# Kernel tuning notes

Hardware: AMD Instinct MI355X
Metric: run time of the kernel (lower is better)

## Reference

```python
import jax, jax.numpy as jnp
import numpy as np

EPS = 1e-5
NH, NS = 8, 4


def layer_norm(x, g, b):
    m = jnp.mean(x, axis=-1, keepdims=True)
    v = jnp.mean((x - m) ** 2, axis=-1, keepdims=True)
    return (x - m) * jax.lax.rsqrt(v + EPS) * g + b


def grid_sample_border(feat, grid):
    # feat: (B,C,H,W), grid: (B,P,S,2) with (x,y) in [-1,1]; bilinear,
    # padding_mode='border', align_corners=True (matches F.grid_sample).
    B, C, H, W = feat.shape
    gx = jnp.clip((grid[..., 0] + 1.0) * 0.5 * (W - 1), 0.0, W - 1.0)
    gy = jnp.clip((grid[..., 1] + 1.0) * 0.5 * (H - 1), 0.0, H - 1.0)
    x0 = jnp.floor(gx)
    y0 = jnp.floor(gy)
    wx = (gx - x0)[:, None]  # (B,1,P,S)
    wy = (gy - y0)[:, None]
    x0i = x0.astype(jnp.int32)
    y0i = y0.astype(jnp.int32)
    x1i = jnp.minimum(x0i + 1, W - 1)
    y1i = jnp.minimum(y0i + 1, H - 1)
    ff = feat.reshape(B, C, H * W)
    gather = jax.vmap(lambda f, i: f[:, i])  # per-batch gather -> (B,C,P,S)
    v00 = gather(ff, y0i * W + x0i)
    v01 = gather(ff, y0i * W + x1i)
    v10 = gather(ff, y1i * W + x0i)
    v11 = gather(ff, y1i * W + x1i)
    return (v00 * (1 - wx) * (1 - wy) + v01 * wx * (1 - wy)
            + v10 * (1 - wx) * wy + v11 * wx * wy)


def setup_inputs() -> dict:
    key = jax.random.key(0)
    ks = jax.random.split(key, 32)
    dim, base = 256, 64
    hd = dim // NH
    inp = {
        'x': jax.random.normal(ks[0], (4, 6, 1024, dim), jnp.float32),
        'ref': jax.random.uniform(ks[1], (4, 1024, 2), jnp.float32) * 2.0 - 1.0,
        'feat0': jax.random.normal(ks[2], (4, base, 128, 128), jnp.float32),
        'feat1': jax.random.normal(ks[3], (4, base * 2, 64, 64), jnp.float32),
        'feat2': jax.random.normal(ks[4], (4, base * 4, 32, 32), jnp.float32),
        'feat3': jax.random.normal(ks[5], (4, base * 8, 16, 16), jnp.float32),
        'feat4': jax.random.normal(ks[6], (4, dim, 16, 16), jnp.float32),
        'norm1_g': jnp.ones((dim,), jnp.float32),
        'norm1_b': jnp.zeros((dim,), jnp.float32),
        'aw_W': 0.02 * jax.random.normal(ks[7], (dim, NH * NS), jnp.float32),
        'aw_b': 0.02 * jax.random.normal(ks[8], (NH * NS,), jnp.float32),
        'so_W': 0.02 * jax.random.normal(ks[9], (dim, 2 * NH * NS), jnp.float32),
        'so_b': 0.1 * jax.random.normal(ks[10], (2 * NH * NS,), jnp.float32),
        'ep0_W': 0.02 * jax.random.normal(ks[11], (base, hd), jnp.float32),
        'ep0_b': jnp.zeros((hd,), jnp.float32),
        'ep1_W': 0.02 * jax.random.normal(ks[12], (base * 2, hd), jnp.float32),
        'ep1_b': jnp.zeros((hd,), jnp.float32),
        'ep2_W': 0.02 * jax.random.normal(ks[13], (base * 4, hd), jnp.float32),
        'ep2_b': jnp.zeros((hd,), jnp.float32),
        'ep3_W': 0.02 * jax.random.normal(ks[14], (base * 8, hd), jnp.float32),
        'ep3_b': jnp.zeros((hd,), jnp.float32),
        'ep4_W': 0.02 * jax.random.normal(ks[15], (dim, hd), jnp.float32),
        'ep4_b': jnp.zeros((hd,), jnp.float32),
        'norm2_g': jnp.ones((dim,), jnp.float32),
        'norm2_b': jnp.zeros((dim,), jnp.float32),
        'fc1_W': 0.02 * jax.random.normal(ks[16], (dim, 2 * dim), jnp.float32),
        'fc1_b': jnp.zeros((2 * dim,), jnp.float32),
        'fc2_W': 0.02 * jax.random.normal(ks[17], (2 * dim, dim), jnp.float32),
        'fc2_b': jnp.zeros((dim,), jnp.float32),
    }
    return inp


def reference(x, ref, feat0, feat1, feat2, feat3, feat4,
              norm1_g, norm1_b, aw_W, aw_b, so_W, so_b,
              ep0_W, ep0_b, ep1_W, ep1_b, ep2_W, ep2_b, ep3_W, ep3_b, ep4_W, ep4_b,
              norm2_g, norm2_b, fc1_W, fc1_b, fc2_W, fc2_b):
    x0_tok, xq = x[:, :1], x[:, 1:]
    b, l, p, c = xq.shape
    hd = c // NH
    residual = xq
    h = layer_norm(xq + x0_tok, norm1_g, norm1_b)
    weights = jax.nn.softmax((h @ aw_W + aw_b).reshape(b, l, p, NH, NS), axis=-1)
    offsets = jnp.tanh((h @ so_W + so_b).reshape(b, l, p, NH * NS, 2))
    pos = offsets + ref[:, None, :, None, :]  # (b,l,p,S,2)
    feats = [feat0, feat1, feat2, feat3, feat4]
    eps_ = [(ep0_W, ep0_b), (ep1_W, ep1_b), (ep2_W, ep2_b), (ep3_W, ep3_b), (ep4_W, ep4_b)]
    sampled = []
    for idx in range(l):
        s = grid_sample_border(feats[idx], pos[:, idx])  # (b,C,p,S)
        s = jnp.transpose(s, (0, 2, 3, 1))                # (b,p,S,C)
        Wp, bp = eps_[idx]
        sampled.append(s @ Wp + bp)                       # (b,p,S,hd)
    fs = jnp.stack(sampled, axis=1).reshape(b, l, p, NH, NS, hd)
    out = jnp.einsum('blphs,blphsd->blphd', weights, fs).reshape(b, l, p, c)
    xq2 = residual + out
    h2 = layer_norm(xq2, norm2_g, norm2_b)
    mlp = jax.nn.gelu(h2 @ fc1_W + fc1_b, approximate=False) @ fc2_W + fc2_b
    xq2 = xq2 + mlp
    return jnp.concatenate([x0_tok, xq2], axis=1)
```

## Files before the change

### kernel.cpp

```cpp
#include <hip/hip_runtime.h>
#include <math.h>

#define B_ 4
#define L_ 5
#define P_ 1024
#define C_ 256
#define TOK (B_ * L_ * P_)

#define PF0_S 0u
#define PF1_S 2097152u
#define PF2_S 2621440u
#define PF3_S 2752512u
#define PF4_S 2785280u
#define WTS_F 1409024u
#define POSS_F 2064384u
#define U_S   0u
#define H1_S  10485760u
#define S_S   15728640u
#define WC_S  17694720u
#define W1T_S 17719296u
#define W2T_S 17850368u
#define BCAT_F 8990720u
#define EWT_S  17981824u

typedef short bf16x8 __attribute__((ext_vector_type(8)));
typedef float f32x4  __attribute__((ext_vector_type(4)));

__device__ __forceinline__ unsigned short f2bf(float f) {
  unsigned u = __float_as_uint(f);
  unsigned r = (u + 0x7fffu + ((u >> 16) & 1u)) >> 16;
  return (unsigned short)r;
}
__device__ __forceinline__ float bf2f(unsigned short u) {
  return __uint_as_float((unsigned)u << 16);
}

__global__ void copy_x0(const float* __restrict__ x, float* __restrict__ out) {
  int i = blockIdx.x * 256 + threadIdx.x;
  int b = i / (P_ * C_);
  int r = i - b * (P_ * C_);
  size_t off = (size_t)b * 6 * P_ * C_ + r;
  out[off] = x[off];
}

__device__ __forceinline__ void block_stats(float v, float* ra, float* rb,
                                            int tid, float* mean, float* var) {
  float a = v, s2 = v * v;
  #pragma unroll
  for (int off = 32; off > 0; off >>= 1) {
    a  += __shfl_xor(a, off);
    s2 += __shfl_xor(s2, off);
  }
  if ((tid & 63) == 0) { ra[tid >> 6] = a; rb[tid >> 6] = s2; }
  __syncthreads();
  float s  = ra[0] + ra[1] + ra[2] + ra[3];
  float ss = rb[0] + rb[1] + rb[2] + rb[3];
  float m = s * (1.0f / C_);
  *mean = m;
  *var = ss * (1.0f / C_) - m * m;
}

__global__ void ln1_h(const float* __restrict__ x,
                      const float* __restrict__ g, const float* __restrict__ bt,
                      unsigned short* __restrict__ h1) {
  __shared__ float ra[4], rb[4];
  int t = blockIdx.x;
  int b = t / (L_ * P_);
  int r = t - b * (L_ * P_);
  int l = r >> 10;
  int p = r & 1023;
  int c = threadIdx.x;
  size_t xq_off = (((size_t)b * 6 + (l + 1)) * P_ + p) * C_;
  size_t x0_off = (((size_t)b * 6) * P_ + p) * C_;
  float v = x[xq_off + c] + x[x0_off + c];
  float mean, var;
  block_stats(v, ra, rb, c, &mean, &var);
  float h = (v - mean) * rsqrtf(var + 1e-5f) * g[c] + bt[c];
  h1[(size_t)t * C_ + c] = f2bf(h);
}

__global__ void ln2_h(const float* __restrict__ out,
                      const float* __restrict__ g, const float* __restrict__ bt,
                      unsigned short* __restrict__ h2) {
  __shared__ float ra[4], rb[4];
  int t = blockIdx.x;
  int b = t / (L_ * P_);
  int r = t - b * (L_ * P_);
  int l = r >> 10;
  int p = r & 1023;
  int c = threadIdx.x;
  size_t o = (((size_t)b * 6 + (l + 1)) * P_ + p) * C_;
  float v = out[o + c];
  float mean, var;
  block_stats(v, ra, rb, c, &mean, &var);
  float h = (v - mean) * rsqrtf(var + 1e-5f) * g[c] + bt[c];
  h2[(size_t)t * C_ + c] = f2bf(h);
}

__global__ void prep_all(const float* __restrict__ f1W, const float* __restrict__ f2W,
                         const float* __restrict__ awW, const float* __restrict__ soW,
                         const float* __restrict__ awb, const float* __restrict__ sob,
                         const float* __restrict__ e0W, const float* __restrict__ e1W,
                         const float* __restrict__ e2W, const float* __restrict__ e3W,
                         const float* __restrict__ e4W,
                         unsigned short* __restrict__ W1T, unsigned short* __restrict__ W2T,
                         unsigned short* __restrict__ Wc, unsigned short* __restrict__ eWT,
                         float* __restrict__ bcat) {
  int i = blockIdx.x * 256 + threadIdx.x;
  if (i < 131072) {
    int n = i >> 8, k = i & 255;
    W1T[i] = f2bf(f1W[k * 512 + n]);
  } else if (i < 262144) {
    int j = i - 131072;
    int n = j >> 9, k = j & 511;
    W2T[j] = f2bf(f2W[k * 256 + n]);
  } else if (i < 286720) {
    int j = i - 262144;
    int n = j >> 8, k = j & 255;
    Wc[j] = f2bf(n < 32 ? awW[k * 32 + n] : soW[k * 64 + (n - 32)]);
  } else if (i < 325632) {
    int j = i - 286720;
    const float* eW; int Cl, base, jj;
    if (j < 2048)       { eW = e0W; Cl = 64;  base = 0;     jj = j; }
    else if (j < 6144)  { eW = e1W; Cl = 128; base = 2048;  jj = j - 2048; }
    else if (j < 14336) { eW = e2W; Cl = 256; base = 6144;  jj = j - 6144; }
    else if (j < 30720) { eW = e3W; Cl = 512; base = 14336; jj = j - 14336; }
    else                { eW = e4W; Cl = 256; base = 30720; jj = j - 30720; }
    int d = jj / Cl, c = jj & (Cl - 1);
    eWT[base + jj] = f2bf(eW[c * 32 + d]);
  } else if (i < 325728) {
    int j = i - 325632;
    bcat[j] = j < 32 ? awb[j] : sob[j - 32];
  }
}

__global__ __launch_bounds__(256) void proj_gemm(
    const float* __restrict__ f0, const float* __restrict__ f1,
    const float* __restrict__ f2, const float* __restrict__ f3,
    const float* __restrict__ f4,
    const unsigned short* __restrict__ eWT,
    unsigned short* __restrict__ pf) {
  constexpr int LDK = 72;
  __shared__ unsigned short Al[64 * LDK];
  __shared__ unsigned short Bl[32 * LDK];
  int blk = blockIdx.x, tid = threadIdx.x;

  const float* feat; int Cl, HW, lt; unsigned pfo, eo;
  if (blk < 1024)      { feat = f0; Cl = 64;  HW = 16384; pfo = PF0_S; eo = 0;     lt = blk; }
  else if (blk < 1280) { feat = f1; Cl = 128; HW = 4096;  pfo = PF1_S; eo = 2048;  lt = blk - 1024; }
  else if (blk < 1344) { feat = f2; Cl = 256; HW = 1024;  pfo = PF2_S; eo = 6144;  lt = blk - 1280; }
  else if (blk < 1360) { feat = f3; Cl = 512; HW = 256;   pfo = PF3_S; eo = 14336; lt = blk - 1344; }
  else                 { feat = f4; Cl = 256; HW = 256;   pfo = PF4_S; eo = 30720; lt = blk - 1360; }
  int tpb = HW >> 6;
  int b = lt / tpb;
  int hw0 = (lt - b * tpb) * 64;
  const float* fb = feat + (size_t)b * Cl * HW;

  int cl = tid & 63, quad = tid >> 6;
  int w = tid >> 6, lane = tid & 63, q = lane >> 4, ml = lane & 15;

  f32x4 acc0 = (f32x4){0.f, 0.f, 0.f, 0.f};
  f32x4 acc1 = (f32x4){0.f, 0.f, 0.f, 0.f};

  for (int k0 = 0; k0 < Cl; k0 += 64) {
    if (k0) __syncthreads();
    { int rr = tid >> 3, kc = (tid & 7) * 8;
      *(int4*)(Bl + rr * LDK + kc) = *(const int4*)(eWT + eo + (size_t)rr * Cl + k0 + kc); }
    const float* src = fb + (size_t)(k0 + cl) * HW + hw0 + quad * 16;
    float4 v0 = *(const float4*)(src);
    float4 v1 = *(const float4*)(src + 4);
    float4 v2 = *(const float4*)(src + 8);
    float4 v3 = *(const float4*)(src + 12);
    unsigned short* ac = Al + cl;
    int mb = quad * 16;
    ac[(mb + 0)  * LDK] = f2bf(v0.x); ac[(mb + 1)  * LDK] = f2bf(v0.y);
    ac[(mb + 2)  * LDK] = f2bf(v0.z); ac[(mb + 3)  * LDK] = f2bf(v0.w);
    ac[(mb + 4)  * LDK] = f2bf(v1.x); ac[(mb + 5)  * LDK] = f2bf(v1.y);
    ac[(mb + 6)  * LDK] = f2bf(v1.z); ac[(mb + 7)  * LDK] = f2bf(v1.w);
    ac[(mb + 8)  * LDK] = f2bf(v2.x); ac[(mb + 9)  * LDK] = f2bf(v2.y);
    ac[(mb + 10) * LDK] = f2bf(v2.z); ac[(mb + 11) * LDK] = f2bf(v2.w);
    ac[(mb + 12) * LDK] = f2bf(v3.x); ac[(mb + 13) * LDK] = f2bf(v3.y);
    ac[(mb + 14) * LDK] = f2bf(v3.z); ac[(mb + 15) * LDK] = f2bf(v3.w);
    __syncthreads();
    #pragma unroll
    for (int ks = 0; ks < 2; ks++) {
      bf16x8 af = *(const bf16x8*)(Al + (w * 16 + ml) * LDK + ks * 32 + q * 8);
      bf16x8 b0 = *(const bf16x8*)(Bl + ml * LDK + ks * 32 + q * 8);
      bf16x8 b1 = *(const bf16x8*)(Bl + (16 + ml) * LDK + ks * 32 + q * 8);
      acc0 = __builtin_amdgcn_mfma_f32_16x16x32_bf16(af, b0, acc0, 0, 0, 0);
      acc1 = __builtin_amdgcn_mfma_f32_16x16x32_bf16(af, b1, acc1, 0, 0, 0);
    }
  }

  #pragma unroll
  for (int nt = 0; nt < 2; nt++) {
    f32x4 a = nt ? acc1 : acc0;
    int d = nt * 16 + ml;
    #pragma unroll
    for (int rr = 0; rr < 4; rr++) {
      int m = w * 16 + q * 4 + rr;
      pf[pfo + ((size_t)b * HW + hw0 + m) * 32 + d] = f2bf(a[rr]);
    }
  }
}

__global__ void postproc(const unsigned short* __restrict__ S, const float* __restrict__ ref,
                         float* __restrict__ wts, float* __restrict__ poss) {
  int t = blockIdx.x;
  int c = threadIdx.x;
  int b = t / (L_ * P_);
  int p = t & (P_ - 1);
  if (c < 32) {
    int g4 = (c >> 2) << 2;
    float s0 = bf2f(S[(size_t)t * 96 + g4 + 0]);
    float s1 = bf2f(S[(size_t)t * 96 + g4 + 1]);
    float s2 = bf2f(S[(size_t)t * 96 + g4 + 2]);
    float s3 = bf2f(S[(size_t)t * 96 + g4 + 3]);
    float m = fmaxf(fmaxf(s0, s1), fmaxf(s2, s3));
    float den = expf(s0 - m) + expf(s1 - m) + expf(s2 - m) + expf(s3 - m);
    float sc = bf2f(S[(size_t)t * 96 + c]);
    wts[(size_t)t * 32 + c] = expf(sc - m) / den;
  } else if (c < 96) {
    int j = c - 32;
    float sv = bf2f(S[(size_t)t * 96 + 32 + j]);
    poss[(size_t)t * 64 + j] = tanhf(sv) + ref[((size_t)b * P_ + p) * 2 + (j & 1)];
  }
}

__global__ __launch_bounds__(256) void sample_comb(
    const float* __restrict__ x, const unsigned short* __restrict__ pf,
    const float* __restrict__ wts, const float* __restrict__ poss,
    const float* __restrict__ e0b, const float* __restrict__ e1b,
    const float* __restrict__ e2b, const float* __restrict__ e3b,
    const float* __restrict__ e4b,
    float* __restrict__ out) {
  __shared__ float coef[512];
  __shared__ int   hwid[512];
  int blk = blockIdx.x;
  int t0 = blk * 4;
  int b = t0 / (L_ * P_);
  int r = t0 - b * (L_ * P_);
  int l = r >> 10;
  int p0 = r & 1023;
  int tid = threadIdx.x;

  int Hl; unsigned pfo; const float* eb;
  if (l == 0)      { Hl = 128; pfo = PF0_S; eb = e0b; }
  else if (l == 1) { Hl = 64;  pfo = PF1_S; eb = e1b; }
  else if (l == 2) { Hl = 32;  pfo = PF2_S; eb = e2b; }
  else if (l == 3) { Hl = 16;  pfo = PF3_S; eb = e3b; }
  else             { Hl = 16;  pfo = PF4_S; eb = e4b; }

  if (tid < 128) {
    int tl = tid >> 5, s = tid & 31;
    int t = t0 + tl;
    float aw = wts[(size_t)t * 32 + s];
    float px = poss[(size_t)t * 64 + s * 2 + 0];
    float py = poss[(size_t)t * 64 + s * 2 + 1];
    float Wm = (float)(Hl - 1);
    float gx = fminf(fmaxf((px + 1.0f) * 0.5f * Wm, 0.0f), Wm);
    float gy = fminf(fmaxf((py + 1.0f) * 0.5f * Wm, 0.0f), Wm);
    float x0f = floorf(gx), y0f = floorf(gy);
    int x0 = (int)x0f, y0 = (int)y0f;
    int x1 = min(x0 + 1, Hl - 1), y1 = min(y0 + 1, Hl - 1);
    float wx = gx - x0f, wy = gy - y0f;
    int base = tid * 4;
    hwid[base + 0] = y0 * Hl + x0; coef[base + 0] = aw * (1.f - wx) * (1.f - wy);
    hwid[base + 1] = y0 * Hl + x1; coef[base + 1] = aw * wx * (1.f - wy);
    hwid[base + 2] = y1 * Hl + x0; coef[base + 2] = aw * (1.f - wx) * wy;
    hwid[base + 3] = y1 * Hl + x1; coef[base + 3] = aw * wx * wy;
  }
  __syncthreads();

  int h = tid >> 5, d = tid & 31;
  const unsigned short* pfb = pf + pfo + (size_t)b * (Hl * Hl) * 32;
  float bv = eb[d];
  #pragma unroll
  for (int tk = 0; tk < 4; ++tk) {
    int cb = tk * 128 + h * 16;
    float acc = 0.f;
    #pragma unroll
    for (int k = 0; k < 16; ++k)
      acc += coef[cb + k] * bf2f(pfb[(size_t)hwid[cb + k] * 32 + d]);
    int p = p0 + tk;
    size_t o = (((size_t)b * 6 + l + 1) * P_ + p) * C_ + h * 32 + d;
    out[o] = x[o] + acc + bv;
  }
}

template<int MODE>
__global__ __launch_bounds__(256) void gemm_bf16(
    const unsigned short* __restrict__ A, const unsigned short* __restrict__ Bt,
    const float* __restrict__ bias, unsigned short* __restrict__ outU,
    float* __restrict__ outF, int N, int K) {
  constexpr int LDK = 72;
  __shared__ unsigned short Al[64 * LDK];
  __shared__ unsigned short Bl[64 * LDK];
  int m0 = blockIdx.x * 64, n0 = blockIdx.y * 64;
  int tid = threadIdx.x;
  int w = tid >> 6, lane = tid & 63;
  int q = lane >> 4, ml = lane & 15;
  int lr = tid >> 3;
  int lk = (tid & 7) * 8;

  f32x4 acc[4];
  #pragma unroll
  for (int i = 0; i < 4; i++) acc[i] = (f32x4){0.f, 0.f, 0.f, 0.f};

  int nr0 = min(n0 + lr, N - 1);
  int nr1 = min(n0 + 32 + lr, N - 1);

  for (int k0 = 0; k0 < K; k0 += 64) {
    int4 a0 = *(const int4*)(A + (size_t)(m0 + lr) * K + k0 + lk);
    int4 a1 = *(const int4*)(A + (size_t)(m0 + 32 + lr) * K + k0 + lk);
    int4 b0 = *(const int4*)(Bt + (size_t)nr0 * K + k0 + lk);
    int4 b1 = *(const int4*)(Bt + (size_t)nr1 * K + k0 + lk);
    __syncthreads();
    *(int4*)(Al + lr * LDK + lk) = a0;
    *(int4*)(Al + (32 + lr) * LDK + lk) = a1;
    *(int4*)(Bl + lr * LDK + lk) = b0;
    *(int4*)(Bl + (32 + lr) * LDK + lk) = b1;
    __syncthreads();
    #pragma unroll
    for (int ks = 0; ks < 2; ks++) {
      bf16x8 af = *(const bf16x8*)(Al + (w * 16 + ml) * LDK + ks * 32 + q * 8);
      #pragma unroll
      for (int nt = 0; nt < 4; nt++) {
        bf16x8 bf = *(const bf16x8*)(Bl + (nt * 16 + ml) * LDK + ks * 32 + q * 8);
        acc[nt] = __builtin_amdgcn_mfma_f32_16x16x32_bf16(af, bf, acc[nt], 0, 0, 0);
      }
    }
  }

  #pragma unroll
  for (int nt = 0; nt < 4; nt++) {
    int n = n0 + nt * 16 + ml;
    if (n >= N) continue;
    float bv = bias[n];
    #pragma unroll
    for (int rr = 0; rr < 4; rr++) {
      int m = m0 + w * 16 + q * 4 + rr;
      float v = acc[nt][rr] + bv;
      if (MODE == 0) {
        v = 0.5f * v * (1.0f + erff(v * 0.70710678118654752f));
        outU[(size_t)m * N + n] = f2bf(v);
      } else if (MODE == 2) {
        outU[(size_t)m * N + n] = f2bf(v);
      } else {
        int s = m >> 10;
        int p = m & 1023;
        int bb = s / 5, ll = s - bb * 5;
        size_t o = (((size_t)bb * 6 + ll + 1) * P_ + p) * C_ + n;
        outF[o] += v;
      }
    }
  }
}

extern "C" void kernel_launch(void* const* d_in, const int* in_sizes, int n_in,
                              void* d_out, int out_size, void* d_ws, size_t ws_size,
                              hipStream_t stream) {
  const float* x     = (const float*)d_in[0];
  const float* ref   = (const float*)d_in[1];
  const float* feat0 = (const float*)d_in[2];
  const float* feat1 = (const float*)d_in[3];
  const float* feat2 = (const float*)d_in[4];
  const float* feat3 = (const float*)d_in[5];
  const float* feat4 = (const float*)d_in[6];
  const float* n1g   = (const float*)d_in[7];
  const float* n1b   = (const float*)d_in[8];
  const float* awW   = (const float*)d_in[9];
  const float* awb   = (const float*)d_in[10];
  const float* soW   = (const float*)d_in[11];
  const float* sob   = (const float*)d_in[12];
  const float* e0W   = (const float*)d_in[13];
  const float* e0b   = (const float*)d_in[14];
  const float* e1W   = (const float*)d_in[15];
  const float* e1b   = (const float*)d_in[16];
  const float* e2W   = (const float*)d_in[17];
  const float* e2b   = (const float*)d_in[18];
  const float* e3W   = (const float*)d_in[19];
  const float* e3b   = (const float*)d_in[20];
  const float* e4W   = (const float*)d_in[21];
  const float* e4b   = (const float*)d_in[22];
  const float* n2g   = (const float*)d_in[23];
  const float* n2b   = (const float*)d_in[24];
  const float* f1W   = (const float*)d_in[25];
  const float* f1b   = (const float*)d_in[26];
  const float* f2W   = (const float*)d_in[27];
  const float* f2b   = (const float*)d_in[28];

  float* wsf = (float*)d_ws;
  unsigned short* ws16 = (unsigned short*)d_ws;
  unsigned short* pf  = ws16;
  float* wts  = wsf + WTS_F;
  float* poss = wsf + POSS_F;
  unsigned short* u   = ws16 + U_S;
  unsigned short* h1  = ws16 + H1_S;
  unsigned short* S   = ws16 + S_S;
  unsigned short* Wc  = ws16 + WC_S;
  unsigned short* W1T = ws16 + W1T_S;
  unsigned short* W2T = ws16 + W2T_S;
  unsigned short* eWT = ws16 + EWT_S;
  float* bcat = wsf + BCAT_F;
  float* out = (float*)d_out;

  prep_all<<<1273, 256, 0, stream>>>(f1W, f2W, awW, soW, awb, sob,
                                     e0W, e1W, e2W, e3W, e4W,
                                     W1T, W2T, Wc, eWT, bcat);

  proj_gemm<<<1376, 256, 0, stream>>>(feat0, feat1, feat2, feat3, feat4, eWT, pf);

  copy_x0<<<(B_ * P_ * C_) / 256, 256, 0, stream>>>(x, out);

  ln1_h<<<TOK, 256, 0, stream>>>(x, n1g, n1b, h1);

  gemm_bf16<2><<<dim3(320, 2), 256, 0, stream>>>(h1, Wc, bcat, S, nullptr, 96, 256);

  postproc<<<TOK, 128, 0, stream>>>(S, ref, wts, poss);

  sample_comb<<<TOK / 4, 256, 0, stream>>>(x, pf, wts, poss,
                                           e0b, e1b, e2b, e3b, e4b, out);

  ln2_h<<<TOK, 256, 0, stream>>>(out, n2g, n2b, h1);

  gemm_bf16<0><<<dim3(320, 8), 256, 0, stream>>>(h1, W1T, f1b, u, nullptr, 512, 256);

  gemm_bf16<1><<<dim3(320, 4), 256, 0, stream>>>(u, W2T, f2b, nullptr, out, 256, 512);
}
```

Baseline: 256.8 us.

## Fuse LN1 with attention projection GEMM and softmax/tanh, and sampling with LN2

```diff
diff --git a/kernel.cpp b/kernel.cpp
--- a/kernel.cpp
+++ b/kernel.cpp
@@ -15,8 +15,7 @@
 #define WTS_F 1409024u
 #define POSS_F 2064384u
 #define U_S   0u
-#define H1_S  10485760u
-#define S_S   15728640u
+#define H2_S  10485760u
 #define WC_S  17694720u
 #define W1T_S 17719296u
 #define W2T_S 17850368u
@@ -35,69 +34,8 @@
   return __uint_as_float((unsigned)u << 16);
 }
 
-__global__ void copy_x0(const float* __restrict__ x, float* __restrict__ out) {
-  int i = blockIdx.x * 256 + threadIdx.x;
-  int b = i / (P_ * C_);
-  int r = i - b * (P_ * C_);
-  size_t off = (size_t)b * 6 * P_ * C_ + r;
-  out[off] = x[off];
-}
-
-__device__ __forceinline__ void block_stats(float v, float* ra, float* rb,
-                                            int tid, float* mean, float* var) {
-  float a = v, s2 = v * v;
-  #pragma unroll
-  for (int off = 32; off > 0; off >>= 1) {
-    a  += __shfl_xor(a, off);
-    s2 += __shfl_xor(s2, off);
-  }
-  if ((tid & 63) == 0) { ra[tid >> 6] = a; rb[tid >> 6] = s2; }
-  __syncthreads();
-  float s  = ra[0] + ra[1] + ra[2] + ra[3];
-  float ss = rb[0] + rb[1] + rb[2] + rb[3];
-  float m = s * (1.0f / C_);
-  *mean = m;
-  *var = ss * (1.0f / C_) - m * m;
-}
-
-__global__ void ln1_h(const float* __restrict__ x,
-                      const float* __restrict__ g, const float* __restrict__ bt,
-                      unsigned short* __restrict__ h1) {
-  __shared__ float ra[4], rb[4];
-  int t = blockIdx.x;
-  int b = t / (L_ * P_);
-  int r = t - b * (L_ * P_);
-  int l = r >> 10;
-  int p = r & 1023;
-  int c = threadIdx.x;
-  size_t xq_off = (((size_t)b * 6 + (l + 1)) * P_ + p) * C_;
-  size_t x0_off = (((size_t)b * 6) * P_ + p) * C_;
-  float v = x[xq_off + c] + x[x0_off + c];
-  float mean, var;
-  block_stats(v, ra, rb, c, &mean, &var);
-  float h = (v - mean) * rsqrtf(var + 1e-5f) * g[c] + bt[c];
-  h1[(size_t)t * C_ + c] = f2bf(h);
-}
-
-__global__ void ln2_h(const float* __restrict__ out,
-                      const float* __restrict__ g, const float* __restrict__ bt,
-                      unsigned short* __restrict__ h2) {
-  __shared__ float ra[4], rb[4];
-  int t = blockIdx.x;
-  int b = t / (L_ * P_);
-  int r = t - b * (L_ * P_);
-  int l = r >> 10;
-  int p = r & 1023;
-  int c = threadIdx.x;
-  size_t o = (((size_t)b * 6 + (l + 1)) * P_ + p) * C_;
-  float v = out[o + c];
-  float mean, var;
-  block_stats(v, ra, rb, c, &mean, &var);
-  float h = (v - mean) * rsqrtf(var + 1e-5f) * g[c] + bt[c];
-  h2[(size_t)t * C_ + c] = f2bf(h);
-}
-
-__global__ void prep_all(const float* __restrict__ f1W, const float* __restrict__ f2W,
+__global__ void prep_all(const float* __restrict__ x, float* __restrict__ out,
+                         const float* __restrict__ f1W, const float* __restrict__ f2W,
                          const float* __restrict__ awW, const float* __restrict__ soW,
                          const float* __restrict__ awb, const float* __restrict__ sob,
                          const float* __restrict__ e0W, const float* __restrict__ e1W,
@@ -107,6 +45,14 @@
                          unsigned short* __restrict__ Wc, unsigned short* __restrict__ eWT,
                          float* __restrict__ bcat) {
   int i = blockIdx.x * 256 + threadIdx.x;
+  if (i < 1048576) {
+    int b = i >> 18;
+    int r = i & 262143;
+    size_t off = (size_t)b * 6 * P_ * C_ + r;
+    out[off] = x[off];
+    return;
+  }
+  i -= 1048576;
   if (i < 131072) {
     int n = i >> 8, k = i & 255;
     W1T[i] = f2bf(f1W[k * 512 + n]);
@@ -204,44 +150,128 @@
   }
 }
 
-__global__ void postproc(const unsigned short* __restrict__ S, const float* __restrict__ ref,
-                         float* __restrict__ wts, float* __restrict__ poss) {
-  int t = blockIdx.x;
-  int c = threadIdx.x;
-  int b = t / (L_ * P_);
-  int p = t & (P_ - 1);
-  if (c < 32) {
-    int g4 = (c >> 2) << 2;
-    float s0 = bf2f(S[(size_t)t * 96 + g4 + 0]);
-    float s1 = bf2f(S[(size_t)t * 96 + g4 + 1]);
-    float s2 = bf2f(S[(size_t)t * 96 + g4 + 2]);
-    float s3 = bf2f(S[(size_t)t * 96 + g4 + 3]);
-    float m = fmaxf(fmaxf(s0, s1), fmaxf(s2, s3));
-    float den = expf(s0 - m) + expf(s1 - m) + expf(s2 - m) + expf(s3 - m);
-    float sc = bf2f(S[(size_t)t * 96 + c]);
-    wts[(size_t)t * 32 + c] = expf(sc - m) / den;
-  } else if (c < 96) {
-    int j = c - 32;
-    float sv = bf2f(S[(size_t)t * 96 + 32 + j]);
-    poss[(size_t)t * 64 + j] = tanhf(sv) + ref[((size_t)b * P_ + p) * 2 + (j & 1)];
-  }
-}
-
-__global__ __launch_bounds__(256) void sample_comb(
+__global__ __launch_bounds__(256) void attn_prep(
+    const float* __restrict__ x, const float* __restrict__ ref,
+    const float* __restrict__ n1g, const float* __restrict__ n1b,
+    const unsigned short* __restrict__ Wc, const float* __restrict__ bcat,
+    float* __restrict__ wts, float* __restrict__ poss) {
+  constexpr int LDA = 264;
+  __shared__ unsigned short Al[64 * LDA];
+  __shared__ unsigned short Bl[96 * 72];
+  __shared__ float gg[C_], bb[C_];
+  int t0 = blockIdx.x * 64;
+  int tid = threadIdx.x;
+
+  gg[tid] = n1g[tid];
+  bb[tid] = n1b[tid];
+  __syncthreads();
+
+  #pragma unroll
+  for (int half = 0; half < 2; ++half) {
+    int r = half * 32 + (tid >> 3);
+    int c0 = (tid & 7) * 32;
+    int t = t0 + r;
+    int b = t / (L_ * P_);
+    int rr_ = t - b * (L_ * P_);
+    int l = rr_ >> 10, p = rr_ & 1023;
+    const float* xq = x + (((size_t)b * 6 + (l + 1)) * P_ + p) * C_ + c0;
+    const float* x0 = x + (((size_t)b * 6) * P_ + p) * C_ + c0;
+    float v[32];
+    float s = 0.f, s2 = 0.f;
+    #pragma unroll
+    for (int i = 0; i < 32; i += 4) {
+      float4 a = *(const float4*)(xq + i);
+      float4 z = *(const float4*)(x0 + i);
+      v[i] = a.x + z.x; v[i + 1] = a.y + z.y; v[i + 2] = a.z + z.z; v[i + 3] = a.w + z.w;
+      s += v[i] + v[i + 1] + v[i + 2] + v[i + 3];
+      s2 += v[i] * v[i] + v[i + 1] * v[i + 1] + v[i + 2] * v[i + 2] + v[i + 3] * v[i + 3];
+    }
+    #pragma unroll
+    for (int off = 1; off < 8; off <<= 1) {
+      s += __shfl_xor(s, off);
+      s2 += __shfl_xor(s2, off);
+    }
+    float mean = s * (1.0f / C_);
+    float var = s2 * (1.0f / C_) - mean * mean;
+    float rs = rsqrtf(var + 1e-5f);
+    unsigned short* dst = Al + r * LDA + c0;
+    #pragma unroll
+    for (int i = 0; i < 32; ++i)
+      dst[i] = f2bf((v[i] - mean) * rs * gg[c0 + i] + bb[c0 + i]);
+  }
+
+  f32x4 acc[6];
+  #pragma unroll
+  for (int i = 0; i < 6; ++i) acc[i] = (f32x4){0.f, 0.f, 0.f, 0.f};
+  int w = tid >> 6, lane = tid & 63, q = lane >> 4, ml = lane & 15;
+
+  for (int k0 = 0; k0 < 256; k0 += 64) {
+    __syncthreads();
+    #pragma unroll
+    for (int i = 0; i < 3; ++i) {
+      int idx = tid + 256 * i;
+      int rw = idx >> 3, kc = (idx & 7) * 8;
+      *(int4*)(Bl + rw * 72 + kc) = *(const int4*)(Wc + (size_t)rw * 256 + k0 + kc);
+    }
+    __syncthreads();
+    #pragma unroll
+    for (int ks = 0; ks < 2; ++ks) {
+      bf16x8 af = *(const bf16x8*)(Al + (w * 16 + ml) * LDA + k0 + ks * 32 + q * 8);
+      #pragma unroll
+      for (int nt = 0; nt < 6; ++nt) {
+        bf16x8 bf = *(const bf16x8*)(Bl + (nt * 16 + ml) * 72 + ks * 32 + q * 8);
+        acc[nt] = __builtin_amdgcn_mfma_f32_16x16x32_bf16(af, bf, acc[nt], 0, 0, 0);
+      }
+    }
+  }
+
+  #pragma unroll
+  for (int nt = 0; nt < 6; ++nt) {
+    int n = nt * 16 + ml;
+    float bv = bcat[n];
+    f32x4 a = acc[nt];
+    if (nt < 2) {
+      #pragma unroll
+      for (int rr = 0; rr < 4; ++rr) {
+        float v = a[rr] + bv;
+        float m1 = fmaxf(v, __shfl_xor(v, 1));
+        float m = fmaxf(m1, __shfl_xor(m1, 2));
+        float e = expf(v - m);
+        float su = e + __shfl_xor(e, 1);
+        su += __shfl_xor(su, 2);
+        int t = t0 + w * 16 + q * 4 + rr;
+        wts[(size_t)t * 32 + n] = e / su;
+      }
+    } else {
+      int j = n - 32;
+      #pragma unroll
+      for (int rr = 0; rr < 4; ++rr) {
+        float v = a[rr] + bv;
+        int t = t0 + w * 16 + q * 4 + rr;
+        int b = t / (L_ * P_);
+        int p = t & 1023;
+        poss[(size_t)t * 64 + j] = tanhf(v) + ref[((size_t)b * P_ + p) * 2 + (j & 1)];
+      }
+    }
+  }
+}
+
+__global__ __launch_bounds__(256) void sample_ln2(
     const float* __restrict__ x, const unsigned short* __restrict__ pf,
     const float* __restrict__ wts, const float* __restrict__ poss,
     const float* __restrict__ e0b, const float* __restrict__ e1b,
     const float* __restrict__ e2b, const float* __restrict__ e3b,
     const float* __restrict__ e4b,
-    float* __restrict__ out) {
-  __shared__ float coef[512];
-  __shared__ int   hwid[512];
-  int blk = blockIdx.x;
-  int t0 = blk * 4;
-  int b = t0 / (L_ * P_);
-  int r = t0 - b * (L_ * P_);
+    const float* __restrict__ n2g, const float* __restrict__ n2b,
+    float* __restrict__ out, unsigned short* __restrict__ h2) {
+  __shared__ float coef[128];
+  __shared__ int   hwid[128];
+  __shared__ float ra[4], rb[4];
+  int t = blockIdx.x;
+  int b = t / (L_ * P_);
+  int r = t - b * (L_ * P_);
   int l = r >> 10;
-  int p0 = r & 1023;
+  int p = r & 1023;
   int tid = threadIdx.x;
 
   int Hl; unsigned pfo; const float* eb;
@@ -251,9 +281,8 @@
   else if (l == 3) { Hl = 16;  pfo = PF3_S; eb = e3b; }
   else             { Hl = 16;  pfo = PF4_S; eb = e4b; }
 
-  if (tid < 128) {
-    int tl = tid >> 5, s = tid & 31;
-    int t = t0 + tl;
+  if (tid < 32) {
+    int s = tid;
     float aw = wts[(size_t)t * 32 + s];
     float px = poss[(size_t)t * 64 + s * 2 + 0];
     float py = poss[(size_t)t * 64 + s * 2 + 1];
@@ -264,7 +293,7 @@
     int x0 = (int)x0f, y0 = (int)y0f;
     int x1 = min(x0 + 1, Hl - 1), y1 = min(y0 + 1, Hl - 1);
     float wx = gx - x0f, wy = gy - y0f;
-    int base = tid * 4;
+    int base = s * 4;
     hwid[base + 0] = y0 * Hl + x0; coef[base + 0] = aw * (1.f - wx) * (1.f - wy);
     hwid[base + 1] = y0 * Hl + x1; coef[base + 1] = aw * wx * (1.f - wy);
     hwid[base + 2] = y1 * Hl + x0; coef[base + 2] = aw * (1.f - wx) * wy;
@@ -274,18 +303,29 @@
 
   int h = tid >> 5, d = tid & 31;
   const unsigned short* pfb = pf + pfo + (size_t)b * (Hl * Hl) * 32;
-  float bv = eb[d];
-  #pragma unroll
-  for (int tk = 0; tk < 4; ++tk) {
-    int cb = tk * 128 + h * 16;
-    float acc = 0.f;
-    #pragma unroll
-    for (int k = 0; k < 16; ++k)
-      acc += coef[cb + k] * bf2f(pfb[(size_t)hwid[cb + k] * 32 + d]);
-    int p = p0 + tk;
-    size_t o = (((size_t)b * 6 + l + 1) * P_ + p) * C_ + h * 32 + d;
-    out[o] = x[o] + acc + bv;
-  }
+  float acc = 0.f;
+  #pragma unroll
+  for (int k = 0; k < 16; ++k)
+    acc += coef[h * 16 + k] * bf2f(pfb[(size_t)hwid[h * 16 + k] * 32 + d]);
+
+  size_t o = (((size_t)b * 6 + l + 1) * P_ + p) * C_ + tid;
+  float v = x[o] + acc + eb[d];
+  out[o] = v;
+
+  float sa = v, s2 = v * v;
+  #pragma unroll
+  for (int off = 32; off > 0; off >>= 1) {
+    sa += __shfl_xor(sa, off);
+    s2 += __shfl_xor(s2, off);
+  }
+  if ((tid & 63) == 0) { ra[tid >> 6] = sa; rb[tid >> 6] = s2; }
+  __syncthreads();
+  float s  = ra[0] + ra[1] + ra[2] + ra[3];
+  float ss = rb[0] + rb[1] + rb[2] + rb[3];
+  float mean = s * (1.0f / C_);
+  float var = ss * (1.0f / C_) - mean * mean;
+  float hh = (v - mean) * rsqrtf(var + 1e-5f) * n2g[tid] + n2b[tid];
+  h2[(size_t)t * C_ + tid] = f2bf(hh);
 }
 
 template<int MODE>
@@ -307,14 +347,11 @@
   #pragma unroll
   for (int i = 0; i < 4; i++) acc[i] = (f32x4){0.f, 0.f, 0.f, 0.f};
 
-  int nr0 = min(n0 + lr, N - 1);
-  int nr1 = min(n0 + 32 + lr, N - 1);
-
   for (int k0 = 0; k0 < K; k0 += 64) {
     int4 a0 = *(const int4*)(A + (size_t)(m0 + lr) * K + k0 + lk);
     int4 a1 = *(const int4*)(A + (size_t)(m0 + 32 + lr) * K + k0 + lk);
-    int4 b0 = *(const int4*)(Bt + (size_t)nr0 * K + k0 + lk);
-    int4 b1 = *(const int4*)(Bt + (size_t)nr1 * K + k0 + lk);
+    int4 b0 = *(const int4*)(Bt + (size_t)(n0 + lr) * K + k0 + lk);
+    int4 b1 = *(const int4*)(Bt + (size_t)(n0 + 32 + lr) * K + k0 + lk);
     __syncthreads();
     *(int4*)(Al + lr * LDK + lk) = a0;
     *(int4*)(Al + (32 + lr) * LDK + lk) = a1;
@@ -335,7 +372,6 @@
   #pragma unroll
   for (int nt = 0; nt < 4; nt++) {
     int n = n0 + nt * 16 + ml;
-    if (n >= N) continue;
     float bv = bias[n];
     #pragma unroll
     for (int rr = 0; rr < 4; rr++) {
@@ -343,8 +379,6 @@
       float v = acc[nt][rr] + bv;
       if (MODE == 0) {
         v = 0.5f * v * (1.0f + erff(v * 0.70710678118654752f));
-        outU[(size_t)m * N + n] = f2bf(v);
-      } else if (MODE == 2) {
         outU[(size_t)m * N + n] = f2bf(v);
       } else {
         int s = m >> 10;
@@ -396,8 +430,7 @@
   float* wts  = wsf + WTS_F;
   float* poss = wsf + POSS_F;
   unsigned short* u   = ws16 + U_S;
-  unsigned short* h1  = ws16 + H1_S;
-  unsigned short* S   = ws16 + S_S;
+  unsigned short* h2  = ws16 + H2_S;
   unsigned short* Wc  = ws16 + WC_S;
   unsigned short* W1T = ws16 + W1T_S;
   unsigned short* W2T = ws16 + W2T_S;
@@ -405,26 +438,19 @@
   float* bcat = wsf + BCAT_F;
   float* out = (float*)d_out;
 
-  prep_all<<<1273, 256, 0, stream>>>(f1W, f2W, awW, soW, awb, sob,
+  prep_all<<<5369, 256, 0, stream>>>(x, out, f1W, f2W, awW, soW, awb, sob,
                                      e0W, e1W, e2W, e3W, e4W,
                                      W1T, W2T, Wc, eWT, bcat);
 
   proj_gemm<<<1376, 256, 0, stream>>>(feat0, feat1, feat2, feat3, feat4, eWT, pf);
 
-  copy_x0<<<(B_ * P_ * C_) / 256, 256, 0, stream>>>(x, out);
-
-  ln1_h<<<TOK, 256, 0, stream>>>(x, n1g, n1b, h1);
-
-  gemm_bf16<2><<<dim3(320, 2), 256, 0, stream>>>(h1, Wc, bcat, S, nullptr, 96, 256);
-
-  postproc<<<TOK, 128, 0, stream>>>(S, ref, wts, poss);
-
-  sample_comb<<<TOK / 4, 256, 0, stream>>>(x, pf, wts, poss,
-                                           e0b, e1b, e2b, e3b, e4b, out);
-
-  ln2_h<<<TOK, 256, 0, stream>>>(out, n2g, n2b, h1);
-
-  gemm_bf16<0><<<dim3(320, 8), 256, 0, stream>>>(h1, W1T, f1b, u, nullptr, 512, 256);
+  attn_prep<<<320, 256, 0, stream>>>(x, ref, n1g, n1b, Wc, bcat, wts, poss);
+
+  sample_ln2<<<TOK, 256, 0, stream>>>(x, pf, wts, poss,
+                                      e0b, e1b, e2b, e3b, e4b,
+                                      n2g, n2b, out, h2);
+
+  gemm_bf16<0><<<dim3(320, 8), 256, 0, stream>>>(h2, W1T, f1b, u, nullptr, 512, 256);
 
   gemm_bf16<1><<<dim3(320, 4), 256, 0, stream>>>(u, W2T, f2b, nullptr, out, 256, 512);
 }
```

Measured after the change: 238.1 us. -7.3%, faster.
